# Kernel optimization log

Measured on AMD Instinct MI355X. Metric: run time of the kernel, lower is better.

Reference implementation:

```python
import jax, jax.numpy as jnp
import numpy as np

N, IN_DIM, HID, HEADS = 4096, 256, 64, 8


def setup_inputs() -> dict:
    key = jax.random.key(0)
    ks = jax.random.split(key, 9)
    feats = jax.random.normal(ks[0], (N, IN_DIM), dtype=jnp.float32)
    adj = jax.random.bernoulli(ks[1], 0.01, (N, N)) | jnp.eye(N, dtype=bool)
    def lin(k, fin, fout):
        return jax.random.normal(k, (fin, fout), dtype=jnp.float32) / np.float32(np.sqrt(fin))
    return {
        "features": feats,
        "adjacency": adj,
        "W_in": lin(ks[2], IN_DIM, HID * HEADS),            # linear (no bias)
        "W_out": lin(ks[3], HID * HEADS, HID),              # out_proj
        "b_out": jnp.zeros((HID,), jnp.float32),
        "W_c1": lin(ks[4], HID * 2, HID),                   # classifier[1]
        "b_c1": jnp.zeros((HID,), jnp.float32),
        "W_c2": lin(ks[5], HID, 1),                         # classifier[3]
        "b_c2": jnp.zeros((1,), jnp.float32),
    }


def reference(features, adjacency, W_in, W_out, b_out, W_c1, b_c1, W_c2, b_c2):
    n = features.shape[0]
    # multi-head GAT: [H, N, D]
    proj = (features @ W_in).reshape(n, HEADS, HID).transpose(1, 0, 2)
    logits = jnp.einsum('hnd,hmd->hnm', proj, proj) / np.float32(np.sqrt(HID))
    logits = jnp.where(adjacency[None, :, :], logits, -jnp.inf)
    attn = jax.nn.softmax(logits, axis=-1)
    attended = jnp.einsum('hnm,hmd->hnd', attn, proj)
    attended = attended.transpose(1, 0, 2).reshape(n, HEADS * HID)
    node_states = attended @ W_out + b_out
    # memory_bank is None -> concat with zeros
    fused = jnp.concatenate([node_states, jnp.zeros_like(node_states)], axis=-1)
    h = jax.nn.gelu(fused, approximate=False) @ W_c1 + b_c1
    scores = (jax.nn.gelu(h, approximate=False) @ W_c2 + b_c2).squeeze(-1)
    # attention heatmap: masked row-normalized cosine similarity
    eps = np.float32(1e-8)
    norm = jnp.maximum(jnp.linalg.norm(node_states, axis=-1, keepdims=True), eps)
    xn = node_states / norm
    sim = jnp.where(adjacency, xn @ xn.T, 0.0)
    heatmap = sim / (sim.sum(axis=-1, keepdims=True) + eps)
    return scores, heatmap
```

## Files before the change

kernel.cpp:

```cpp
#include <hip/hip_runtime.h>
#include <math.h>

constexpr int NN    = 4096;
constexpr int INDIM = 256;
constexpr int HID   = 64;
constexpr int HEADS = 8;
constexpr int HH    = HID * HEADS;
constexpr int DMAX  = 256;

typedef float        vfloat4 __attribute__((ext_vector_type(4)));
typedef unsigned int vuint4  __attribute__((ext_vector_type(4)));

__device__ __forceinline__ float gelu_exact(float x) {
    return 0.5f * x * (1.0f + erff(x * 0.70710678118654752f));
}

__device__ __forceinline__ float wave_reduce64(float v) {
    v += __shfl_xor(v, 32); v += __shfl_xor(v, 16); v += __shfl_xor(v, 8);
    v += __shfl_xor(v, 4);  v += __shfl_xor(v, 2);  v += __shfl_xor(v, 1);
    return v;
}

__global__ void detect_kernel(const unsigned int* __restrict__ adj, int* __restrict__ flag) {
    __shared__ int sawU8;
    int t = threadIdx.x;
    if (t == 0) sawU8 = 0;
    __syncthreads();
    int u8 = 0;
    for (int i = t; i < 4096; i += 256) {
        unsigned int w = adj[i];
        if (((w & ~0x01010101u) == 0u) && ((w & 0xFFFFFF00u) != 0u)) u8 = 1;
    }
    if (u8) atomicOr(&sawU8, 1);
    __syncthreads();
    if (t == 0) flag[0] = sawU8 ? 1 : 0;
}

__global__ __launch_bounds__(256) void csr_kernel(
    const void* __restrict__ adjv, const int* __restrict__ flag,
    unsigned short* __restrict__ nbr_g, int* __restrict__ deg_g) {
    __shared__ int wsum[4];
    const int n = blockIdx.x, t = threadIdx.x;
    const int wv = t >> 6, lane = t & 63;

    unsigned int nzmask = 0;
    if (flag[0] == 1) {
        const vuint4* src = reinterpret_cast<const vuint4*>(
            (const unsigned char*)adjv + (size_t)n * NN + 16 * t);
        const vuint4 r = __builtin_nontemporal_load(src);
        #pragma unroll
        for (int a = 0; a < 4; ++a)
            #pragma unroll
            for (int j = 0; j < 4; ++j)
                if ((r[a] >> (8 * j)) & 0xFFu) nzmask |= 1u << (a * 4 + j);
    } else {
        const vuint4* p = reinterpret_cast<const vuint4*>(
            (const unsigned int*)adjv + (size_t)n * NN + 16 * t);
        #pragma unroll
        for (int a = 0; a < 4; ++a) {
            const vuint4 r = __builtin_nontemporal_load(p + a);
            if (r[0]) nzmask |= 1u << (a * 4 + 0);
            if (r[1]) nzmask |= 1u << (a * 4 + 1);
            if (r[2]) nzmask |= 1u << (a * 4 + 2);
            if (r[3]) nzmask |= 1u << (a * 4 + 3);
        }
    }
    const int c = __popc(nzmask);
    int x = c;
    #pragma unroll
    for (int d = 1; d < 64; d <<= 1) {
        int y = __shfl_up(x, d);
        if (lane >= d) x += y;
    }
    if (lane == 63) wsum[wv] = x;
    __syncthreads();
    int base = 0;
    #pragma unroll
    for (int i = 0; i < 4; ++i)
        if (i < wv) base += wsum[i];
    const int deg = min(wsum[0] + wsum[1] + wsum[2] + wsum[3], DMAX);
    if (t == 0) deg_g[n] = deg;
    int o = base + x - c;
    unsigned int mm = nzmask;
    while (mm) {
        const int j = __ffs(mm) - 1;
        mm &= mm - 1;
        if (o < DMAX) nbr_g[(size_t)n * DMAX + o] = (unsigned short)(16 * t + j);
        ++o;
    }
}

__global__ __launch_bounds__(256) void proj_kernel(const float* __restrict__ A,
                                                   const float* __restrict__ B,
                                                   float* __restrict__ projT) {
    __shared__ float Bs[INDIM][64];
    const int bx = blockIdx.x, by = blockIdx.y, t = threadIdx.x;
    const int tx = t & 15, ty = t >> 4;

    #pragma unroll
    for (int i = t; i < INDIM * 16; i += 256) {
        const int k = i >> 4, c4 = (i & 15) * 4;
        *reinterpret_cast<float4*>(&Bs[k][c4]) =
            *reinterpret_cast<const float4*>(B + (size_t)k * HH + bx * 64 + c4);
    }
    __syncthreads();

    const float* ap0 = A + (size_t)(by * 64 + ty * 4 + 0) * INDIM;
    const float* ap1 = A + (size_t)(by * 64 + ty * 4 + 1) * INDIM;
    const float* ap2 = A + (size_t)(by * 64 + ty * 4 + 2) * INDIM;
    const float* ap3 = A + (size_t)(by * 64 + ty * 4 + 3) * INDIM;

    float acc[4][4] = {{0.0f}};
    #pragma unroll 2
    for (int k = 0; k < INDIM; k += 4) {
        float4 av[4];
        av[0] = *reinterpret_cast<const float4*>(ap0 + k);
        av[1] = *reinterpret_cast<const float4*>(ap1 + k);
        av[2] = *reinterpret_cast<const float4*>(ap2 + k);
        av[3] = *reinterpret_cast<const float4*>(ap3 + k);
        float4 bv[4];
        #pragma unroll
        for (int kk = 0; kk < 4; ++kk)
            bv[kk] = *reinterpret_cast<const float4*>(&Bs[k + kk][tx * 4]);
        #pragma unroll
        for (int i = 0; i < 4; ++i) {
            const float a0 = av[i].x, a1 = av[i].y, a2 = av[i].z, a3 = av[i].w;
            acc[i][0] += a0 * bv[0].x + a1 * bv[1].x + a2 * bv[2].x + a3 * bv[3].x;
            acc[i][1] += a0 * bv[0].y + a1 * bv[1].y + a2 * bv[2].y + a3 * bv[3].y;
            acc[i][2] += a0 * bv[0].z + a1 * bv[1].z + a2 * bv[2].z + a3 * bv[3].z;
            acc[i][3] += a0 * bv[0].w + a1 * bv[1].w + a2 * bv[2].w + a3 * bv[3].w;
        }
    }
    #pragma unroll
    for (int i = 0; i < 4; ++i) {
        float4 o = {acc[i][0], acc[i][1], acc[i][2], acc[i][3]};
        *reinterpret_cast<float4*>(
            projT + ((size_t)bx * NN + by * 64 + ty * 4 + i) * HID + tx * 4) = o;
    }
}

__global__ __launch_bounds__(256) void attn_kernel(
    const float* __restrict__ projT,
    const unsigned short* __restrict__ nbr_g, const int* __restrict__ deg_g,
    float* __restrict__ attended) {
    __shared__ unsigned short nl[4][DMAX];
    const int b = blockIdx.x, t = threadIdx.x;
    const int wv = t >> 6, lane = t & 63;
    const int h = b & 7;
    const int n = (b >> 3) * 4 + wv;
    const int deg = deg_g[n];

    *reinterpret_cast<ushort4*>(&nl[wv][lane * 4]) =
        *reinterpret_cast<const ushort4*>(nbr_g + (size_t)n * DMAX + lane * 4);

    const float* tab = projT + (size_t)h * NN * HID;
    const int g = lane >> 3, dl = (lane & 7) * 8;

    float q[8];
    {
        const float4 a = *reinterpret_cast<const float4*>(tab + (size_t)n * HID + dl);
        const float4 bq = *reinterpret_cast<const float4*>(tab + (size_t)n * HID + dl + 4);
        q[0] = a.x;  q[1] = a.y;  q[2] = a.z;  q[3] = a.w;
        q[4] = bq.x; q[5] = bq.y; q[6] = bq.z; q[7] = bq.w;
    }

    float l = 0.0f;
    float acc[8] = {0.f, 0.f, 0.f, 0.f, 0.f, 0.f, 0.f, 0.f};
    for (int c0 = 0; c0 < deg; c0 += 8) {
        const int c = c0 + g;
        const int idx = nl[wv][min(c, deg - 1)];
        const float* kp = tab + (size_t)idx * HID + dl;
        const float4 ka = *reinterpret_cast<const float4*>(kp);
        const float4 kb = *reinterpret_cast<const float4*>(kp + 4);
        float kf[8] = {ka.x, ka.y, ka.z, ka.w, kb.x, kb.y, kb.z, kb.w};
        float s = q[0]*kf[0] + q[1]*kf[1] + q[2]*kf[2] + q[3]*kf[3] +
                  q[4]*kf[4] + q[5]*kf[5] + q[6]*kf[6] + q[7]*kf[7];
        s += __shfl_xor(s, 1); s += __shfl_xor(s, 2); s += __shfl_xor(s, 4);
        const float w = (c < deg) ? expf(s * 0.125f) : 0.0f;
        l += w;
        #pragma unroll
        for (int i = 0; i < 8; ++i) acc[i] += w * kf[i];
    }
    l += __shfl_xor(l, 8); l += __shfl_xor(l, 16); l += __shfl_xor(l, 32);
    #pragma unroll
    for (int i = 0; i < 8; ++i) {
        acc[i] += __shfl_xor(acc[i], 8);
        acc[i] += __shfl_xor(acc[i], 16);
        acc[i] += __shfl_xor(acc[i], 32);
    }
    const float invL = 1.0f / l;
    if (g == 0) {
        float4 o1 = {acc[0] * invL, acc[1] * invL, acc[2] * invL, acc[3] * invL};
        float4 o2 = {acc[4] * invL, acc[5] * invL, acc[6] * invL, acc[7] * invL};
        float* dst = attended + (size_t)n * HH + h * HID + dl;
        *reinterpret_cast<float4*>(dst)     = o1;
        *reinterpret_cast<float4*>(dst + 4) = o2;
    }
}

__global__ __launch_bounds__(256) void post_kernel(
    const float* __restrict__ attended,
    const float* __restrict__ W_out, const float* __restrict__ b_out,
    const float* __restrict__ W_c1, const float* __restrict__ b_c1,
    const float* __restrict__ W_c2, const float* __restrict__ b_c2,
    float* __restrict__ scores, float* __restrict__ xn) {
    __shared__ float qv2[4][HH];
    __shared__ float red[4][256];
    __shared__ float nsbuf[4][HID];
    const int n0 = blockIdx.x * 4, t = threadIdx.x;
    const int wv = t >> 6, lane = t & 63;

    #pragma unroll
    for (int nd = 0; nd < 4; ++nd) {
        qv2[nd][t]       = attended[(size_t)(n0 + nd) * HH + t];
        qv2[nd][t + 256] = attended[(size_t)(n0 + nd) * HH + t + 256];
    }
    __syncthreads();

    const int j = t & 63, part = t >> 6;
    float p0 = 0.f, p1 = 0.f, p2 = 0.f, p3 = 0.f;
    for (int d = part * 128; d < part * 128 + 128; ++d) {
        const float w = W_out[d * HID + j];
        p0 += qv2[0][d] * w; p1 += qv2[1][d] * w;
        p2 += qv2[2][d] * w; p3 += qv2[3][d] * w;
    }
    red[0][t] = p0; red[1][t] = p1; red[2][t] = p2; red[3][t] = p3;
    __syncthreads();
    if (wv < 4 && lane < HID) {
        nsbuf[wv][lane] = red[wv][lane] + red[wv][lane + 64] +
                          red[wv][lane + 128] + red[wv][lane + 192] + b_out[lane];
    }
    __syncthreads();

    const int n = n0 + wv;
    const float ns = nsbuf[wv][lane];
    const float s2 = wave_reduce64(ns * ns);
    const float invn = 1.0f / fmaxf(sqrtf(s2), 1e-8f);
    xn[(size_t)n * HID + lane] = ns * invn;
    const float gb = gelu_exact(ns);
    __syncthreads();
    nsbuf[wv][lane] = gb;
    float hv = b_c1[lane];
    for (int i = 0; i < HID; ++i) hv += nsbuf[wv][i] * W_c1[i * HID + lane];
    const float hb = gelu_exact(hv);
    const float sc_ = wave_reduce64(hb * W_c2[lane]);
    if (lane == 0) scores[n] = sc_ + b_c2[0];
}

__global__ __launch_bounds__(256, 8) void heat_kernel(
    const unsigned short* __restrict__ nbr_g, const int* __restrict__ deg_g,
    const float* __restrict__ xn, float* __restrict__ heat) {
    __shared__ float srow[NN];
    __shared__ float simv[DMAX];
    __shared__ unsigned short nl[DMAX];
    __shared__ float inv_s;
    const int n = blockIdx.x, t = threadIdx.x;
    const int wv = t >> 6, lane = t & 63;
    const int deg = deg_g[n];

    float4* sr4 = (float4*)srow;
    const float4 z4 = {0.f, 0.f, 0.f, 0.f};
    for (int i = t; i < NN / 4; i += 256) sr4[i] = z4;
    if (t < deg) nl[t] = nbr_g[(size_t)n * DMAX + t];
    const float xq = xn[(size_t)n * HID + lane];
    __syncthreads();

    for (int c = wv; c < deg; c += 4) {
        const int m = nl[c];
        float s = wave_reduce64(xq * xn[(size_t)m * HID + lane]);
        if (lane == 0) { srow[m] = s; simv[c] = s; }
    }
    __syncthreads();
    if (t < 64) {
        float ps = 0.0f;
        for (int c = t; c < deg; c += 64) ps += simv[c];
        ps = wave_reduce64(ps);
        if (t == 0) inv_s = 1.0f / (ps + 1e-8f);
    }
    __syncthreads();
    const float inv = inv_s;
    vfloat4* hr4 = (vfloat4*)(heat + (size_t)n * NN);
    for (int i = t; i < NN / 4; i += 256) {
        float4 v = sr4[i];
        vfloat4 nv = {v.x * inv, v.y * inv, v.z * inv, v.w * inv};
        __builtin_nontemporal_store(nv, hr4 + i);
    }
}

extern "C" void kernel_launch(void* const* d_in, const int* in_sizes, int n_in,
                              void* d_out, int out_size, void* d_ws, size_t ws_size,
                              hipStream_t stream) {
    const float* features = (const float*)d_in[0];
    const void*  adj      = d_in[1];
    const float* W_in     = (const float*)d_in[2];
    const float* W_out    = (const float*)d_in[3];
    const float* b_out    = (const float*)d_in[4];
    const float* W_c1     = (const float*)d_in[5];
    const float* b_c1     = (const float*)d_in[6];
    const float* W_c2     = (const float*)d_in[7];
    const float* b_c2     = (const float*)d_in[8];

    float* scores = (float*)d_out;
    float* heat   = (float*)d_out + NN;

    float*          projT    = (float*)d_ws;
    float*          attended = projT + (size_t)HEADS * NN * HID;
    float*          xn       = attended + (size_t)NN * HH;
    unsigned short* nbr_g    = (unsigned short*)(xn + (size_t)NN * HID);
    int*            deg_g    = (int*)(nbr_g + (size_t)NN * DMAX);
    int*            flag     = deg_g + NN;

    detect_kernel<<<1, 256, 0, stream>>>((const unsigned int*)adj, flag);
    csr_kernel<<<NN, 256, 0, stream>>>(adj, flag, nbr_g, deg_g);
    proj_kernel<<<dim3(HH / 64, NN / 64), 256, 0, stream>>>(features, W_in, projT);
    attn_kernel<<<NN * HEADS / 4, 256, 0, stream>>>(projT, nbr_g, deg_g, attended);
    post_kernel<<<NN / 4, 256, 0, stream>>>(attended, W_out, b_out, W_c1, b_c1,
                                            W_c2, b_c2, scores, xn);
    heat_kernel<<<NN, 256, 0, stream>>>(nbr_g, deg_g, xn, heat);
}
```

Before: 222.9 us.

## Fuse dtype detection, CSR build and projection GEMM into one prep kernel

Merges the three front kernels (adjacency dtype detection, CSR neighbor-list construction, input projection GEMM) into a single launch whose blocks are split by index between the GEMM tiles and the per-row CSR work. Each CSR block redoes the dtype check on the first 4 KB of the adjacency instead of depending on a separate one-block kernel. The GEMM's shared B tile is halved and staged in two K chunks to cut LDS use and allow more resident blocks. The aim is to remove two launches and their serialization and let the compute-bound GEMM overlap the bandwidth-bound adjacency scan. The cost is a redundant 4 KB read per CSR block, and CSR blocks now reserve the GEMM's shared memory even though they do not use it.

```diff
diff --git a/kernel.cpp b/kernel.cpp
--- a/kernel.cpp
+++ b/kernel.cpp
@@ -7,6 +7,7 @@
 constexpr int HEADS = 8;
 constexpr int HH    = HID * HEADS;
 constexpr int DMAX  = 256;
+constexpr int PROJ_BLOCKS = 512;
 
 typedef float        vfloat4 __attribute__((ext_vector_type(4)));
 typedef unsigned int vuint4  __attribute__((ext_vector_type(4)));
@@ -21,121 +22,123 @@
     return v;
 }
 
-__global__ void detect_kernel(const unsigned int* __restrict__ adj, int* __restrict__ flag) {
-    __shared__ int sawU8;
-    int t = threadIdx.x;
-    if (t == 0) sawU8 = 0;
-    __syncthreads();
-    int u8 = 0;
-    for (int i = t; i < 4096; i += 256) {
-        unsigned int w = adj[i];
-        if (((w & ~0x01010101u) == 0u) && ((w & 0xFFFFFF00u) != 0u)) u8 = 1;
-    }
-    if (u8) atomicOr(&sawU8, 1);
-    __syncthreads();
-    if (t == 0) flag[0] = sawU8 ? 1 : 0;
-}
-
-__global__ __launch_bounds__(256) void csr_kernel(
-    const void* __restrict__ adjv, const int* __restrict__ flag,
+__global__ __launch_bounds__(256) void prep_kernel(
+    const void* __restrict__ adjv,
+    const float* __restrict__ A, const float* __restrict__ B,
+    float* __restrict__ projT,
     unsigned short* __restrict__ nbr_g, int* __restrict__ deg_g) {
-    __shared__ int wsum[4];
-    const int n = blockIdx.x, t = threadIdx.x;
+    __shared__ float Bs[128][64];
+    __shared__ int wsum[4], u8w[4];
+    const int pb = blockIdx.x, t = threadIdx.x;
     const int wv = t >> 6, lane = t & 63;
 
-    unsigned int nzmask = 0;
-    if (flag[0] == 1) {
-        const vuint4* src = reinterpret_cast<const vuint4*>(
-            (const unsigned char*)adjv + (size_t)n * NN + 16 * t);
-        const vuint4 r = __builtin_nontemporal_load(src);
-        #pragma unroll
-        for (int a = 0; a < 4; ++a)
+    if (pb < PROJ_BLOCKS) {
+        const int bx = pb & 7, by = pb >> 3;
+        const int tx = t & 15, ty = t >> 4;
+        const float* ap0 = A + (size_t)(by * 64 + ty * 4 + 0) * INDIM;
+        const float* ap1 = A + (size_t)(by * 64 + ty * 4 + 1) * INDIM;
+        const float* ap2 = A + (size_t)(by * 64 + ty * 4 + 2) * INDIM;
+        const float* ap3 = A + (size_t)(by * 64 + ty * 4 + 3) * INDIM;
+        float acc[4][4] = {{0.0f}};
+
+        for (int kh = 0; kh < 2; ++kh) {
             #pragma unroll
-            for (int j = 0; j < 4; ++j)
-                if ((r[a] >> (8 * j)) & 0xFFu) nzmask |= 1u << (a * 4 + j);
+            for (int i = t; i < 128 * 16; i += 256) {
+                const int k = i >> 4, c4 = (i & 15) * 4;
+                *reinterpret_cast<float4*>(&Bs[k][c4]) =
+                    *reinterpret_cast<const float4*>(
+                        B + (size_t)(kh * 128 + k) * HH + bx * 64 + c4);
+            }
+            __syncthreads();
+            #pragma unroll 2
+            for (int k = 0; k < 128; k += 4) {
+                const int ka = kh * 128 + k;
+                float4 av[4];
+                av[0] = *reinterpret_cast<const float4*>(ap0 + ka);
+                av[1] = *reinterpret_cast<const float4*>(ap1 + ka);
+                av[2] = *reinterpret_cast<const float4*>(ap2 + ka);
+                av[3] = *reinterpret_cast<const float4*>(ap3 + ka);
+                float4 bv[4];
+                #pragma unroll
+                for (int kk = 0; kk < 4; ++kk)
+                    bv[kk] = *reinterpret_cast<const float4*>(&Bs[k + kk][tx * 4]);
+                #pragma unroll
+                for (int i = 0; i < 4; ++i) {
+                    const float a0 = av[i].x, a1 = av[i].y, a2 = av[i].z, a3 = av[i].w;
+                    acc[i][0] += a0 * bv[0].x + a1 * bv[1].x + a2 * bv[2].x + a3 * bv[3].x;
+                    acc[i][1] += a0 * bv[0].y + a1 * bv[1].y + a2 * bv[2].y + a3 * bv[3].y;
+                    acc[i][2] += a0 * bv[0].z + a1 * bv[1].z + a2 * bv[2].z + a3 * bv[3].z;
+                    acc[i][3] += a0 * bv[0].w + a1 * bv[1].w + a2 * bv[2].w + a3 * bv[3].w;
+                }
+            }
+            __syncthreads();
+        }
+        #pragma unroll
+        for (int i = 0; i < 4; ++i) {
+            float4 o = {acc[i][0], acc[i][1], acc[i][2], acc[i][3]};
+            *reinterpret_cast<float4*>(
+                projT + ((size_t)bx * NN + by * 64 + ty * 4 + i) * HID + tx * 4) = o;
+        }
     } else {
-        const vuint4* p = reinterpret_cast<const vuint4*>(
-            (const unsigned int*)adjv + (size_t)n * NN + 16 * t);
+        const int n = pb - PROJ_BLOCKS;
+        const vuint4 pw = __builtin_nontemporal_load(
+            reinterpret_cast<const vuint4*>(adjv) + t);
+        int u8loc = 0;
         #pragma unroll
         for (int a = 0; a < 4; ++a) {
-            const vuint4 r = __builtin_nontemporal_load(p + a);
-            if (r[0]) nzmask |= 1u << (a * 4 + 0);
-            if (r[1]) nzmask |= 1u << (a * 4 + 1);
-            if (r[2]) nzmask |= 1u << (a * 4 + 2);
-            if (r[3]) nzmask |= 1u << (a * 4 + 3);
-        }
-    }
-    const int c = __popc(nzmask);
-    int x = c;
-    #pragma unroll
-    for (int d = 1; d < 64; d <<= 1) {
-        int y = __shfl_up(x, d);
-        if (lane >= d) x += y;
-    }
-    if (lane == 63) wsum[wv] = x;
-    __syncthreads();
-    int base = 0;
-    #pragma unroll
-    for (int i = 0; i < 4; ++i)
-        if (i < wv) base += wsum[i];
-    const int deg = min(wsum[0] + wsum[1] + wsum[2] + wsum[3], DMAX);
-    if (t == 0) deg_g[n] = deg;
-    int o = base + x - c;
-    unsigned int mm = nzmask;
-    while (mm) {
-        const int j = __ffs(mm) - 1;
-        mm &= mm - 1;
-        if (o < DMAX) nbr_g[(size_t)n * DMAX + o] = (unsigned short)(16 * t + j);
-        ++o;
-    }
-}
-
-__global__ __launch_bounds__(256) void proj_kernel(const float* __restrict__ A,
-                                                   const float* __restrict__ B,
-                                                   float* __restrict__ projT) {
-    __shared__ float Bs[INDIM][64];
-    const int bx = blockIdx.x, by = blockIdx.y, t = threadIdx.x;
-    const int tx = t & 15, ty = t >> 4;
-
-    #pragma unroll
-    for (int i = t; i < INDIM * 16; i += 256) {
-        const int k = i >> 4, c4 = (i & 15) * 4;
-        *reinterpret_cast<float4*>(&Bs[k][c4]) =
-            *reinterpret_cast<const float4*>(B + (size_t)k * HH + bx * 64 + c4);
-    }
-    __syncthreads();
-
-    const float* ap0 = A + (size_t)(by * 64 + ty * 4 + 0) * INDIM;
-    const float* ap1 = A + (size_t)(by * 64 + ty * 4 + 1) * INDIM;
-    const float* ap2 = A + (size_t)(by * 64 + ty * 4 + 2) * INDIM;
-    const float* ap3 = A + (size_t)(by * 64 + ty * 4 + 3) * INDIM;
-
-    float acc[4][4] = {{0.0f}};
-    #pragma unroll 2
-    for (int k = 0; k < INDIM; k += 4) {
-        float4 av[4];
-        av[0] = *reinterpret_cast<const float4*>(ap0 + k);
-        av[1] = *reinterpret_cast<const float4*>(ap1 + k);
-        av[2] = *reinterpret_cast<const float4*>(ap2 + k);
-        av[3] = *reinterpret_cast<const float4*>(ap3 + k);
-        float4 bv[4];
-        #pragma unroll
-        for (int kk = 0; kk < 4; ++kk)
-            bv[kk] = *reinterpret_cast<const float4*>(&Bs[k + kk][tx * 4]);
-        #pragma unroll
-        for (int i = 0; i < 4; ++i) {
-            const float a0 = av[i].x, a1 = av[i].y, a2 = av[i].z, a3 = av[i].w;
-            acc[i][0] += a0 * bv[0].x + a1 * bv[1].x + a2 * bv[2].x + a3 * bv[3].x;
-            acc[i][1] += a0 * bv[0].y + a1 * bv[1].y + a2 * bv[2].y + a3 * bv[3].y;
-            acc[i][2] += a0 * bv[0].z + a1 * bv[1].z + a2 * bv[2].z + a3 * bv[3].z;
-            acc[i][3] += a0 * bv[0].w + a1 * bv[1].w + a2 * bv[2].w + a3 * bv[3].w;
-        }
-    }
-    #pragma unroll
-    for (int i = 0; i < 4; ++i) {
-        float4 o = {acc[i][0], acc[i][1], acc[i][2], acc[i][3]};
-        *reinterpret_cast<float4*>(
-            projT + ((size_t)bx * NN + by * 64 + ty * 4 + i) * HID + tx * 4) = o;
+            const unsigned w = pw[a];
+            if (((w & ~0x01010101u) == 0u) && ((w & 0xFFFFFF00u) != 0u)) u8loc = 1;
+        }
+        const unsigned long long wb = __ballot(u8loc);
+        if (lane == 0) u8w[wv] = (wb != 0ull);
+        __syncthreads();
+        const bool isU8 = (u8w[0] | u8w[1] | u8w[2] | u8w[3]) != 0;
+
+        unsigned int nzmask = 0;
+        if (isU8) {
+            const vuint4 r = __builtin_nontemporal_load(
+                reinterpret_cast<const vuint4*>(
+                    (const unsigned char*)adjv + (size_t)n * NN + 16 * t));
+            #pragma unroll
+            for (int a = 0; a < 4; ++a)
+                #pragma unroll
+                for (int j = 0; j < 4; ++j)
+                    if ((r[a] >> (8 * j)) & 0xFFu) nzmask |= 1u << (a * 4 + j);
+        } else {
+            const vuint4* p = reinterpret_cast<const vuint4*>(
+                (const unsigned int*)adjv + (size_t)n * NN + 16 * t);
+            #pragma unroll
+            for (int a = 0; a < 4; ++a) {
+                const vuint4 r = __builtin_nontemporal_load(p + a);
+                if (r[0]) nzmask |= 1u << (a * 4 + 0);
+                if (r[1]) nzmask |= 1u << (a * 4 + 1);
+                if (r[2]) nzmask |= 1u << (a * 4 + 2);
+                if (r[3]) nzmask |= 1u << (a * 4 + 3);
+            }
+        }
+        const int c = __popc(nzmask);
+        int x = c;
+        #pragma unroll
+        for (int d = 1; d < 64; d <<= 1) {
+            int y = __shfl_up(x, d);
+            if (lane >= d) x += y;
+        }
+        if (lane == 63) wsum[wv] = x;
+        __syncthreads();
+        int base = 0;
+        #pragma unroll
+        for (int i = 0; i < 4; ++i)
+            if (i < wv) base += wsum[i];
+        const int deg = min(wsum[0] + wsum[1] + wsum[2] + wsum[3], DMAX);
+        if (t == 0) deg_g[n] = deg;
+        int o = base + x - c;
+        unsigned int mm = nzmask;
+        while (mm) {
+            const int j = __ffs(mm) - 1;
+            mm &= mm - 1;
+            if (o < DMAX) nbr_g[(size_t)n * DMAX + o] = (unsigned short)(16 * t + j);
+            ++o;
+        }
     }
 }
 
@@ -308,11 +311,9 @@
     float*          xn       = attended + (size_t)NN * HH;
     unsigned short* nbr_g    = (unsigned short*)(xn + (size_t)NN * HID);
     int*            deg_g    = (int*)(nbr_g + (size_t)NN * DMAX);
-    int*            flag     = deg_g + NN;
-
-    detect_kernel<<<1, 256, 0, stream>>>((const unsigned int*)adj, flag);
-    csr_kernel<<<NN, 256, 0, stream>>>(adj, flag, nbr_g, deg_g);
-    proj_kernel<<<dim3(HH / 64, NN / 64), 256, 0, stream>>>(features, W_in, projT);
+
+    prep_kernel<<<PROJ_BLOCKS + NN, 256, 0, stream>>>(adj, features, W_in,
+                                                      projT, nbr_g, deg_g);
     attn_kernel<<<NN * HEADS / 4, 256, 0, stream>>>(projT, nbr_g, deg_g, attended);
     post_kernel<<<NN / 4, 256, 0, stream>>>(attended, W_out, b_out, W_c1, b_c1,
                                             W_c2, b_c2, scores, xn);
```

After: 211.8 us. 1.05x faster.
